# Performance work log

Measured on AMD Instinct MI355X. Metric: run time of the kernel, lower is better.

Reference implementation:

```python
import jax, jax.numpy as jnp
import numpy as np

B, S, E, H = 16, 512, 768, 12
D = E // H
SCALING = 1.0 / np.sqrt(D * 1.0)  # scaling_factor = 1


def setup_inputs() -> dict:
    key = jax.random.key(0)
    ks = jax.random.split(key, 8)
    query = jax.random.normal(ks[0], (B, S, E), dtype=jnp.float32)
    key_in = jax.random.normal(ks[1], (B, S, E), dtype=jnp.float32)
    value = jax.random.normal(ks[2], (B, S, E), dtype=jnp.float32)
    key_padding_mask = jax.random.randint(ks[3], (B, S), 0, 2).astype(jnp.bool_)
    attn_bias = jax.random.normal(ks[4], (B, H, S, S), dtype=jnp.float32)
    # Learned params. NOTE: original code applies wq to q, k AND v (wk/wv unused).
    Wq = jax.random.normal(ks[5], (E, E), dtype=jnp.float32) * (1.0 / np.sqrt(E))
    bq = jnp.zeros((E,), dtype=jnp.float32)
    Wo = jax.random.normal(ks[6], (E, E), dtype=jnp.float32) * (1.0 / np.sqrt(E))
    bo = jnp.zeros((E,), dtype=jnp.float32)
    return {"query": query, "key": key_in, "value": value,
            "key_padding_mask": key_padding_mask, "attn_bias": attn_bias,
            "Wq": Wq, "bq": bq, "Wo": Wo, "bo": bo}


def _split_heads(x):
    # [B,S,E] -> [B,H,S,D]
    return x.reshape(B, S, H, D).transpose(0, 2, 1, 3)


def reference(query, key, value, key_padding_mask, attn_bias, Wq, bq, Wo, bo):
    q = (query @ Wq + bq) * jnp.asarray(SCALING, query.dtype)
    k = key @ Wq + bq      # faithful: wq used for k and v in the source
    v = value @ Wq + bq
    q, k, v = _split_heads(q), _split_heads(k), _split_heads(v)  # [B,H,S,D]
    w = jnp.einsum('bhtd,bhsd->bhts', q, k)                      # [B,H,T,S]
    w = jnp.where(key_padding_mask[:, None, None, :], -jnp.inf, w)
    w = w + attn_bias
    attn = jax.nn.softmax(w, axis=-1)  # dropout is no-op (training=False)
    o = jnp.einsum('bhts,bhsd->bhtd', attn, v)
    o = o.transpose(0, 2, 1, 3).reshape(B, S, E)
    o = o @ Wo + bo
    attn_weights = w.reshape(B * H, S, S)
    return (o, attn_weights, attn.reshape(B * H, S, S))
```

## Files before the change

### kernel.cpp

```cpp
#include <hip/hip_runtime.h>
#include <cmath>

#define BB 16
#define SS 512
#define EE 768
#define HH 12
#define DD 64
#define NBH (BB*HH)

#define MASK_NEG (-1.0e30f)

__device__ __forceinline__ unsigned short bf16_rn(float x) {
    unsigned u = __float_as_uint(x);
    u += 0x7FFFu + ((u >> 16) & 1u);
    return (unsigned short)(u >> 16);
}
__device__ __forceinline__ float bf16_tof(unsigned short h) {
    return __uint_as_float(((unsigned)h) << 16);
}

typedef __attribute__((ext_vector_type(8))) short bf16x8;
typedef __attribute__((ext_vector_type(4))) float f32x4;
typedef __attribute__((ext_vector_type(4))) unsigned short u16x4;

__global__ __launch_bounds__(256) void conv_w_kernel(
    const float* __restrict__ Wq, const float* __restrict__ Wo,
    unsigned short* __restrict__ wtq, unsigned short* __restrict__ wto)
{
    const float* __restrict__ W = blockIdx.z ? Wo : Wq;
    unsigned short* __restrict__ wt = blockIdx.z ? wto : wtq;
    const int k = blockIdx.x * 256 + threadIdx.x;
    const int n = blockIdx.y;
    const float x = W[(size_t)k * EE + n];
    const unsigned short h = bf16_rn(x);
    const float r = x - bf16_tof(h);
    const unsigned short m = bf16_rn(r);
    const float l2 = r - bf16_tof(m);
    const unsigned short l = bf16_rn(l2);
    const size_t PL = (size_t)EE * EE;
    wt[0 * PL + (size_t)n * EE + k] = h;
    wt[1 * PL + (size_t)n * EE + k] = m;
    wt[2 * PL + (size_t)n * EE + k] = l;
}

__global__ __launch_bounds__(256) void split_gemm_qkv_kernel(
    const float* __restrict__ Xq, const float* __restrict__ Xk,
    const float* __restrict__ Xv, const unsigned short* __restrict__ wt,
    const float* __restrict__ bvec,
    unsigned short* __restrict__ qp, unsigned short* __restrict__ kp,
    unsigned short* __restrict__ vtp)
{
    const int z = blockIdx.z;
    const float* __restrict__ X = (z == 1) ? Xk : (z == 2) ? Xv : Xq;
    const float scale = (z == 0) ? 0.125f : 1.0f;

    const int m0 = blockIdx.x * 128;
    const int n0 = blockIdx.y * 128;

    __shared__ __align__(16) unsigned short lds[4 * 4096];
    const int AH = 0, AL = 4096, BH = 8192, BL = 12288;

    const int tid = threadIdx.x;
    const int srow = tid >> 2;
    const int sg   = tid & 3;
    const int wv = tid >> 6;
    const int wr = wv >> 1, wc = wv & 1;
    const int lane = tid & 63;
    const int l15 = lane & 15, lg = lane >> 4;

    const size_t PL = (size_t)EE * EE;
    const size_t PS = (size_t)NBH * SS * DD;

    f32x4 acc[4][4];
#pragma unroll
    for (int i = 0; i < 4; ++i)
#pragma unroll
        for (int j = 0; j < 4; ++j) acc[i][j] = (f32x4){0.f, 0.f, 0.f, 0.f};

#pragma unroll 1
    for (int k0 = 0; k0 < EE; k0 += 32) {
#pragma unroll
        for (int half = 0; half < 2; ++half) {
            const int row = srow + 64 * half;
            const float* xp = &X[(size_t)(m0 + row) * EE + k0 + sg * 8];
            const float4 f0 = *reinterpret_cast<const float4*>(xp);
            const float4 f1 = *reinterpret_cast<const float4*>(xp + 4);
            const float xs[8] = {f0.x, f0.y, f0.z, f0.w, f1.x, f1.y, f1.z, f1.w};
            bf16x8 hv, mv;
#pragma unroll
            for (int e = 0; e < 8; ++e) {
                const float x = xs[e];
                const unsigned short h = bf16_rn(x);
                const unsigned short m = bf16_rn(x - bf16_tof(h));
                hv[e] = (short)h;
                mv[e] = (short)m;
            }
            const int o = row * 32 + sg * 8;
            *reinterpret_cast<bf16x8*>(&lds[AH + o]) = hv;
            *reinterpret_cast<bf16x8*>(&lds[AL + o]) = mv;

            const size_t bo = (size_t)(n0 + row) * EE + k0 + sg * 8;
            *reinterpret_cast<bf16x8*>(&lds[BH + o]) =
                *reinterpret_cast<const bf16x8*>(&wt[0 * PL + bo]);
            *reinterpret_cast<bf16x8*>(&lds[BL + o]) =
                *reinterpret_cast<const bf16x8*>(&wt[1 * PL + bo]);
        }
        __syncthreads();

        bf16x8 ah[4], al[4];
#pragma unroll
        for (int i = 0; i < 4; ++i) {
            const int o = (wr * 64 + i * 16 + l15) * 32 + lg * 8;
            ah[i] = *reinterpret_cast<const bf16x8*>(&lds[AH + o]);
            al[i] = *reinterpret_cast<const bf16x8*>(&lds[AL + o]);
        }
#pragma unroll
        for (int j = 0; j < 4; ++j) {
            const int o = (wc * 64 + j * 16 + l15) * 32 + lg * 8;
            const bf16x8 bh = *reinterpret_cast<const bf16x8*>(&lds[BH + o]);
            const bf16x8 bl = *reinterpret_cast<const bf16x8*>(&lds[BL + o]);
#pragma unroll
            for (int i = 0; i < 4; ++i) {
                acc[i][j] = __builtin_amdgcn_mfma_f32_16x16x32_bf16(ah[i], bh, acc[i][j], 0, 0, 0);
                acc[i][j] = __builtin_amdgcn_mfma_f32_16x16x32_bf16(ah[i], bl, acc[i][j], 0, 0, 0);
                acc[i][j] = __builtin_amdgcn_mfma_f32_16x16x32_bf16(al[i], bh, acc[i][j], 0, 0, 0);
                acc[i][j] = __builtin_amdgcn_mfma_f32_16x16x32_bf16(al[i], bl, acc[i][j], 0, 0, 0);
            }
        }
        __syncthreads();
    }

    unsigned short* __restrict__ dstp = (z == 0) ? qp : kp;
#pragma unroll
    for (int j = 0; j < 4; ++j) {
        const int n = n0 + wc * 64 + j * 16 + l15;
        const float bvn = bvec[n];
        const int h = n >> 6, d = n & 63;
#pragma unroll
        for (int i = 0; i < 4; ++i) {
            const int mb = m0 + wr * 64 + i * 16 + lg * 4;
#pragma unroll
            for (int r = 0; r < 4; ++r) {
                const int m = mb + r;
                const int bh_ = (m >> 9) * HH + h;
                const int srow_ = m & 511;
                const float val = (acc[i][j][r] + bvn) * scale;
                const unsigned short hi = bf16_rn(val);
                const unsigned short lo = bf16_rn(val - bf16_tof(hi));
                if (z == 2) {
                    const size_t o = ((size_t)bh_ * DD + d) * SS + srow_;
                    vtp[o] = hi;
                    vtp[o + PS] = lo;
                } else {
                    const size_t o = ((size_t)bh_ * SS + srow_) * DD + d;
                    dstp[o] = hi;
                    dstp[o + PS] = lo;
                }
            }
        }
    }
}

__global__ __launch_bounds__(256) void flash_attn_kernel(
    const unsigned short* __restrict__ qp, const unsigned short* __restrict__ kp,
    const unsigned short* __restrict__ vt, const unsigned char* __restrict__ mask,
    const float* __restrict__ bias, float* __restrict__ wout,
    float* __restrict__ ohb, float* __restrict__ stat_m,
    float* __restrict__ stat_inv)
{
    const int bh = blockIdx.y;
    const int b = bh / HH, h = bh % HH;
    const int t0 = blockIdx.x * 64;
    const int tid = threadIdx.x;
    const int wv = tid >> 6;
    const int lane = tid & 63, l15 = lane & 15, lg = lane >> 4;
    const size_t PS = (size_t)NBH * SS * DD;

    __shared__ __align__(16) unsigned short kbuf[2 * 64 * 68];
    __shared__ __align__(16) unsigned short vbuf[2 * 64 * 68];
    __shared__ __align__(16) unsigned short pbuf[4 * 2 * 16 * 68];

    bf16x8 bqh[2], bql[2];
    {
        const unsigned short* qbase = &qp[((size_t)bh * SS + t0 + wv * 16) * DD];
#pragma unroll
        for (int kc = 0; kc < 2; ++kc) {
            const size_t o = (size_t)l15 * DD + kc * 32 + lg * 8;
            bqh[kc] = *reinterpret_cast<const bf16x8*>(&qbase[o]);
            bql[kc] = *reinterpret_cast<const bf16x8*>(&qbase[o + PS]);
        }
    }

    float rm = -3.0e38f, rs = 0.0f;

    f32x4 oac[4];
#pragma unroll
    for (int j = 0; j < 4; ++j) oac[j] = (f32x4){0.f, 0.f, 0.f, 0.f};

    const int t = t0 + wv * 16 + l15;

#pragma unroll 1
    for (int c = 0; c < 8; ++c) {
        const int sc = c * 64;
        __syncthreads();

        const unsigned short* kbase = &kp[((size_t)bh * SS + sc) * DD];
        const unsigned short* vbase = &vt[(size_t)bh * DD * SS + sc];
#pragma unroll
        for (int rep = 0; rep < 2; ++rep) {
            const int row = (tid >> 3) + rep * 32;
            const int g = (tid & 7) * 8;
            *reinterpret_cast<bf16x8*>(&kbuf[row * 68 + g]) =
                *reinterpret_cast<const bf16x8*>(&kbase[(size_t)row * DD + g]);
            *reinterpret_cast<bf16x8*>(&kbuf[64 * 68 + row * 68 + g]) =
                *reinterpret_cast<const bf16x8*>(&kbase[(size_t)row * DD + g + PS]);
            *reinterpret_cast<bf16x8*>(&vbuf[row * 68 + g]) =
                *reinterpret_cast<const bf16x8*>(&vbase[(size_t)row * SS + g]);
            *reinterpret_cast<bf16x8*>(&vbuf[64 * 68 + row * 68 + g]) =
                *reinterpret_cast<const bf16x8*>(&vbase[(size_t)row * SS + g + PS]);
        }
        __syncthreads();

        f32x4 ws[4];
#pragma unroll
        for (int i = 0; i < 4; ++i) ws[i] = (f32x4){0.f, 0.f, 0.f, 0.f};
#pragma unroll
        for (int kc = 0; kc < 2; ++kc) {
#pragma unroll
            for (int i = 0; i < 4; ++i) {
                const int o = (i * 16 + l15) * 68 + kc * 32 + lg * 8;
                const bf16x8 ah = *reinterpret_cast<const bf16x8*>(&kbuf[o]);
                const bf16x8 al = *reinterpret_cast<const bf16x8*>(&kbuf[64 * 68 + o]);
                ws[i] = __builtin_amdgcn_mfma_f32_16x16x32_bf16(ah, bqh[kc], ws[i], 0, 0, 0);
                ws[i] = __builtin_amdgcn_mfma_f32_16x16x32_bf16(ah, bql[kc], ws[i], 0, 0, 0);
                ws[i] = __builtin_amdgcn_mfma_f32_16x16x32_bf16(al, bqh[kc], ws[i], 0, 0, 0);
                ws[i] = __builtin_amdgcn_mfma_f32_16x16x32_bf16(al, bql[kc], ws[i], 0, 0, 0);
            }
        }

        float mx = -3.0e38f;
#pragma unroll
        for (int i = 0; i < 4; ++i) {
            const int s = sc + i * 16 + lg * 4;
            const size_t go = ((size_t)bh * SS + t) * SS + s;
            const float4 bv = *reinterpret_cast<const float4*>(&bias[go]);
            const uchar4 mk = *reinterpret_cast<const uchar4*>(&mask[b * SS + s]);
            float4 w4;
            w4.x = mk.x ? MASK_NEG : ws[i][0] + bv.x;
            w4.y = mk.y ? MASK_NEG : ws[i][1] + bv.y;
            w4.z = mk.z ? MASK_NEG : ws[i][2] + bv.z;
            w4.w = mk.w ? MASK_NEG : ws[i][3] + bv.w;
            *reinterpret_cast<float4*>(&wout[go]) = w4;
            ws[i][0] = w4.x; ws[i][1] = w4.y; ws[i][2] = w4.z; ws[i][3] = w4.w;
            mx = fmaxf(mx, fmaxf(fmaxf(w4.x, w4.y), fmaxf(w4.z, w4.w)));
        }
        mx = fmaxf(mx, __shfl_xor(mx, 16));
        mx = fmaxf(mx, __shfl_xor(mx, 32));

        const float m_new = fmaxf(rm, mx);
        float sm = 0.0f;
#pragma unroll
        for (int i = 0; i < 4; ++i)
#pragma unroll
            for (int r = 0; r < 4; ++r) sm += __expf(ws[i][r] - m_new);
        sm += __shfl_xor(sm, 16);
        sm += __shfl_xor(sm, 32);
        const float scl = __expf(rm - m_new);
        rs = rs * scl + sm;
        rm = m_new;

        unsigned short* pw = &pbuf[(wv * 2) * 16 * 68];
#pragma unroll
        for (int i = 0; i < 4; ++i) {
            float4 p4;
            p4.x = __expf(ws[i][0] - m_new);
            p4.y = __expf(ws[i][1] - m_new);
            p4.z = __expf(ws[i][2] - m_new);
            p4.w = __expf(ws[i][3] - m_new);
            u16x4 hv, lv;
            hv.x = bf16_rn(p4.x); lv.x = bf16_rn(p4.x - bf16_tof(hv.x));
            hv.y = bf16_rn(p4.y); lv.y = bf16_rn(p4.y - bf16_tof(hv.y));
            hv.z = bf16_rn(p4.z); lv.z = bf16_rn(p4.z - bf16_tof(hv.z));
            hv.w = bf16_rn(p4.w); lv.w = bf16_rn(p4.w - bf16_tof(hv.w));
            const int po = l15 * 68 + i * 16 + lg * 4;
            *reinterpret_cast<u16x4*>(&pw[po]) = hv;
            *reinterpret_cast<u16x4*>(&pw[16 * 68 + po]) = lv;
        }

        float sclr[4];
#pragma unroll
        for (int r = 0; r < 4; ++r) sclr[r] = __shfl(scl, lg * 4 + r);
#pragma unroll
        for (int j = 0; j < 4; ++j)
#pragma unroll
            for (int r = 0; r < 4; ++r) oac[j][r] *= sclr[r];

#pragma unroll
        for (int kc = 0; kc < 2; ++kc) {
            const int ko = kc * 32 + lg * 8;
            const bf16x8 pah = *reinterpret_cast<const bf16x8*>(&pw[l15 * 68 + ko]);
            const bf16x8 pal = *reinterpret_cast<const bf16x8*>(&pw[16 * 68 + l15 * 68 + ko]);
#pragma unroll
            for (int j = 0; j < 4; ++j) {
                const int o = (j * 16 + l15) * 68 + ko;
                const bf16x8 vh = *reinterpret_cast<const bf16x8*>(&vbuf[o]);
                const bf16x8 vl = *reinterpret_cast<const bf16x8*>(&vbuf[64 * 68 + o]);
                oac[j] = __builtin_amdgcn_mfma_f32_16x16x32_bf16(pah, vh, oac[j], 0, 0, 0);
                oac[j] = __builtin_amdgcn_mfma_f32_16x16x32_bf16(pah, vl, oac[j], 0, 0, 0);
                oac[j] = __builtin_amdgcn_mfma_f32_16x16x32_bf16(pal, vh, oac[j], 0, 0, 0);
                oac[j] = __builtin_amdgcn_mfma_f32_16x16x32_bf16(pal, vl, oac[j], 0, 0, 0);
            }
        }
    }

    const float inv = 1.0f / rs;
    if (lg == 0) {
        stat_m[(size_t)bh * SS + t] = rm;
        stat_inv[(size_t)bh * SS + t] = inv;
    }
    float invr[4];
#pragma unroll
    for (int r = 0; r < 4; ++r) invr[r] = __shfl(inv, lg * 4 + r);
#pragma unroll
    for (int j = 0; j < 4; ++j)
#pragma unroll
        for (int r = 0; r < 4; ++r) {
            const int tr = t0 + wv * 16 + lg * 4 + r;
            ohb[((size_t)b * SS + tr) * EE + h * DD + j * 16 + l15] = oac[j][r] * invr[r];
        }
}

__global__ __launch_bounds__(256) void finish_kernel(
    const float* __restrict__ X, const unsigned short* __restrict__ wt,
    const float* __restrict__ bvec, float* __restrict__ dflat,
    const float* __restrict__ win, const float* __restrict__ stat_m,
    const float* __restrict__ stat_inv, float* __restrict__ attn)
{
    __shared__ __align__(16) unsigned short lds[6 * 4096];

    if (blockIdx.x >= 384) {
        const int nb = gridDim.x - 384;
        const size_t total = (size_t)NBH * SS * (SS / 4);
        for (size_t g = (size_t)(blockIdx.x - 384) * 256 + threadIdx.x; g < total;
             g += (size_t)nb * 256) {
            const size_t row = g >> 7;
            const float m_ = stat_m[row];
            const float iv = stat_inv[row];
            const float4 w4 = reinterpret_cast<const float4*>(win)[g];
            float4 p4;
            p4.x = __expf(w4.x - m_) * iv;
            p4.y = __expf(w4.y - m_) * iv;
            p4.z = __expf(w4.z - m_) * iv;
            p4.w = __expf(w4.w - m_) * iv;
            reinterpret_cast<float4*>(attn)[g] = p4;
        }
        return;
    }

    const int m0 = (blockIdx.x & 63) * 128;
    const int n0 = (blockIdx.x >> 6) * 128;

    const int AH = 0, AM = 4096, AL = 8192, BH = 12288, BM = 16384, BL = 20480;

    const int tid = threadIdx.x;
    const int srow = tid >> 2;
    const int sg   = tid & 3;
    const int wv = tid >> 6;
    const int wr = wv >> 1, wc = wv & 1;
    const int lane = tid & 63;
    const int l15 = lane & 15, lg = lane >> 4;
    const size_t PL = (size_t)EE * EE;

    f32x4 acc[4][4];
#pragma unroll
    for (int i = 0; i < 4; ++i)
#pragma unroll
        for (int j = 0; j < 4; ++j) acc[i][j] = (f32x4){0.f, 0.f, 0.f, 0.f};

#pragma unroll 1
    for (int k0 = 0; k0 < EE; k0 += 32) {
#pragma unroll
        for (int half = 0; half < 2; ++half) {
            const int row = srow + 64 * half;
            const float* xp = &X[(size_t)(m0 + row) * EE + k0 + sg * 8];
            const float4 f0 = *reinterpret_cast<const float4*>(xp);
            const float4 f1 = *reinterpret_cast<const float4*>(xp + 4);
            const float xs[8] = {f0.x, f0.y, f0.z, f0.w, f1.x, f1.y, f1.z, f1.w};
            bf16x8 hv, mv, lv;
#pragma unroll
            for (int e = 0; e < 8; ++e) {
                const float x = xs[e];
                const unsigned short h = bf16_rn(x);
                const float r = x - bf16_tof(h);
                const unsigned short m = bf16_rn(r);
                const float l2 = r - bf16_tof(m);
                hv[e] = (short)h;
                mv[e] = (short)m;
                lv[e] = (short)bf16_rn(l2);
            }
            const int o = row * 32 + sg * 8;
            *reinterpret_cast<bf16x8*>(&lds[AH + o]) = hv;
            *reinterpret_cast<bf16x8*>(&lds[AM + o]) = mv;
            *reinterpret_cast<bf16x8*>(&lds[AL + o]) = lv;

            const size_t bo = (size_t)(n0 + row) * EE + k0 + sg * 8;
            *reinterpret_cast<bf16x8*>(&lds[BH + o]) =
                *reinterpret_cast<const bf16x8*>(&wt[0 * PL + bo]);
            *reinterpret_cast<bf16x8*>(&lds[BM + o]) =
                *reinterpret_cast<const bf16x8*>(&wt[1 * PL + bo]);
            *reinterpret_cast<bf16x8*>(&lds[BL + o]) =
                *reinterpret_cast<const bf16x8*>(&wt[2 * PL + bo]);
        }
        __syncthreads();

        bf16x8 ah[4], am[4], al[4];
#pragma unroll
        for (int i = 0; i < 4; ++i) {
            const int o = (wr * 64 + i * 16 + l15) * 32 + lg * 8;
            ah[i] = *reinterpret_cast<const bf16x8*>(&lds[AH + o]);
            am[i] = *reinterpret_cast<const bf16x8*>(&lds[AM + o]);
            al[i] = *reinterpret_cast<const bf16x8*>(&lds[AL + o]);
        }
#pragma unroll
        for (int j = 0; j < 4; ++j) {
            const int o = (wc * 64 + j * 16 + l15) * 32 + lg * 8;
            const bf16x8 bh = *reinterpret_cast<const bf16x8*>(&lds[BH + o]);
            const bf16x8 bm = *reinterpret_cast<const bf16x8*>(&lds[BM + o]);
            const bf16x8 bl = *reinterpret_cast<const bf16x8*>(&lds[BL + o]);
#pragma unroll
            for (int i = 0; i < 4; ++i) {
                acc[i][j] = __builtin_amdgcn_mfma_f32_16x16x32_bf16(ah[i], bh, acc[i][j], 0, 0, 0);
                acc[i][j] = __builtin_amdgcn_mfma_f32_16x16x32_bf16(ah[i], bm, acc[i][j], 0, 0, 0);
                acc[i][j] = __builtin_amdgcn_mfma_f32_16x16x32_bf16(am[i], bh, acc[i][j], 0, 0, 0);
                acc[i][j] = __builtin_amdgcn_mfma_f32_16x16x32_bf16(ah[i], bl, acc[i][j], 0, 0, 0);
                acc[i][j] = __builtin_amdgcn_mfma_f32_16x16x32_bf16(al[i], bh, acc[i][j], 0, 0, 0);
                acc[i][j] = __builtin_amdgcn_mfma_f32_16x16x32_bf16(am[i], bm, acc[i][j], 0, 0, 0);
            }
        }
        __syncthreads();
    }

#pragma unroll
    for (int j = 0; j < 4; ++j) {
        const int n = n0 + wc * 64 + j * 16 + l15;
        const float bvn = bvec[n];
#pragma unroll
        for (int i = 0; i < 4; ++i) {
            const int mb = m0 + wr * 64 + i * 16 + lg * 4;
#pragma unroll
            for (int r = 0; r < 4; ++r)
                dflat[(size_t)(mb + r) * EE + n] = acc[i][j][r] + bvn;
        }
    }
}

__global__ __launch_bounds__(256) void proj_kernel(
    const float* __restrict__ Xq, const float* __restrict__ Xk,
    const float* __restrict__ Xv, const float* __restrict__ W,
    const float* __restrict__ bvec, float* __restrict__ qb,
    float* __restrict__ kb, float* __restrict__ vb)
{
    const int z = blockIdx.z;
    const float* __restrict__ X = (z == 0) ? Xq : (z == 1) ? Xk : Xv;
    float* __restrict__ Dst = (z == 0) ? qb : (z == 1) ? kb : vb;
    const float scale = (z == 0) ? 0.125f : 1.0f;

    const int m0 = blockIdx.x * 128;
    const int n0 = blockIdx.y * 128;

    __shared__ float As[16][128];
    __shared__ float Bs[16][128];

    const int tid = threadIdx.x;
    const int ty = tid >> 4, tx = tid & 15;

    float acc[8][8];
#pragma unroll
    for (int i = 0; i < 8; ++i)
#pragma unroll
        for (int j = 0; j < 8; ++j) acc[i][j] = 0.0f;

    const int arow = tid >> 1;
    const int ak   = (tid & 1) * 8;
    const int brow = tid >> 4;
    const int bn   = (tid & 15) * 8;

    for (int k0 = 0; k0 < EE; k0 += 16) {
        const float4* ap = reinterpret_cast<const float4*>(&X[(size_t)(m0 + arow) * EE + k0 + ak]);
        float4 a0 = ap[0], a1 = ap[1];
        As[ak + 0][arow] = a0.x; As[ak + 1][arow] = a0.y;
        As[ak + 2][arow] = a0.z; As[ak + 3][arow] = a0.w;
        As[ak + 4][arow] = a1.x; As[ak + 5][arow] = a1.y;
        As[ak + 6][arow] = a1.z; As[ak + 7][arow] = a1.w;

        const float4* bp = reinterpret_cast<const float4*>(&W[(size_t)(k0 + brow) * EE + n0 + bn]);
        float4 b0 = bp[0], b1 = bp[1];
        *reinterpret_cast<float4*>(&Bs[brow][bn])     = b0;
        *reinterpret_cast<float4*>(&Bs[brow][bn + 4]) = b1;
        __syncthreads();

#pragma unroll
        for (int kk = 0; kk < 16; ++kk) {
            float4 aA = *reinterpret_cast<const float4*>(&As[kk][ty * 8]);
            float4 aB = *reinterpret_cast<const float4*>(&As[kk][ty * 8 + 4]);
            float4 bA = *reinterpret_cast<const float4*>(&Bs[kk][tx * 8]);
            float4 bB = *reinterpret_cast<const float4*>(&Bs[kk][tx * 8 + 4]);
            float av[8] = {aA.x, aA.y, aA.z, aA.w, aB.x, aB.y, aB.z, aB.w};
            float bv[8] = {bA.x, bA.y, bA.z, bA.w, bB.x, bB.y, bB.z, bB.w};
#pragma unroll
            for (int i = 0; i < 8; ++i)
#pragma unroll
                for (int j = 0; j < 8; ++j)
                    acc[i][j] = fmaf(av[i], bv[j], acc[i][j]);
        }
        __syncthreads();
    }

    const int nbase = n0 + tx * 8;
    float bq8[8];
    {
        float4 c0 = *reinterpret_cast<const float4*>(&bvec[nbase]);
        float4 c1 = *reinterpret_cast<const float4*>(&bvec[nbase + 4]);
        bq8[0]=c0.x; bq8[1]=c0.y; bq8[2]=c0.z; bq8[3]=c0.w;
        bq8[4]=c1.x; bq8[5]=c1.y; bq8[6]=c1.z; bq8[7]=c1.w;
    }
    const int hh = nbase >> 6;
    const int dd = nbase & 63;
#pragma unroll
    for (int i = 0; i < 8; ++i) {
        const int m = m0 + ty * 8 + i;
        const int bidx = m >> 9;
        const int srow = m & 511;
        float* dst = &Dst[(((size_t)bidx * HH + hh) * SS + srow) * DD + dd];
        float4 v0, v1;
        v0.x = (acc[i][0] + bq8[0]) * scale;
        v0.y = (acc[i][1] + bq8[1]) * scale;
        v0.z = (acc[i][2] + bq8[2]) * scale;
        v0.w = (acc[i][3] + bq8[3]) * scale;
        v1.x = (acc[i][4] + bq8[4]) * scale;
        v1.y = (acc[i][5] + bq8[5]) * scale;
        v1.z = (acc[i][6] + bq8[6]) * scale;
        v1.w = (acc[i][7] + bq8[7]) * scale;
        *reinterpret_cast<float4*>(dst)     = v0;
        *reinterpret_cast<float4*>(dst + 4) = v1;
    }
}

__global__ __launch_bounds__(256) void scores_kernel(
    const float* __restrict__ qb, const float* __restrict__ kb,
    const unsigned char* __restrict__ mask,
    const float* __restrict__ bias, float* __restrict__ wout)
{
    const int bh = blockIdx.z;
    const int b  = bh / HH;
    const int t0 = blockIdx.y * 128;
    const int s0 = blockIdx.x * 128;

    __shared__ float As[16][128];
    __shared__ float Bs[16][128];

    const int tid = threadIdx.x;
    const int ty = tid >> 4, tx = tid & 15;

    float acc[8][8];
#pragma unroll
    for (int i = 0; i < 8; ++i)
#pragma unroll
        for (int j = 0; j < 8; ++j) acc[i][j] = 0.0f;

    const int arow = tid >> 1;
    const int ak   = (tid & 1) * 8;

    const float* __restrict__ qbase = &qb[(size_t)bh * SS * DD];
    const float* __restrict__ kbase = &kb[(size_t)bh * SS * DD];

    for (int k0 = 0; k0 < DD; k0 += 16) {
        const float4* ap = reinterpret_cast<const float4*>(&qbase[(size_t)(t0 + arow) * DD + k0 + ak]);
        float4 a0 = ap[0], a1 = ap[1];
        As[ak + 0][arow] = a0.x; As[ak + 1][arow] = a0.y;
        As[ak + 2][arow] = a0.z; As[ak + 3][arow] = a0.w;
        As[ak + 4][arow] = a1.x; As[ak + 5][arow] = a1.y;
        As[ak + 6][arow] = a1.z; As[ak + 7][arow] = a1.w;

        const float4* bp = reinterpret_cast<const float4*>(&kbase[(size_t)(s0 + arow) * DD + k0 + ak]);
        float4 b0 = bp[0], b1 = bp[1];
        Bs[ak + 0][arow] = b0.x; Bs[ak + 1][arow] = b0.y;
        Bs[ak + 2][arow] = b0.z; Bs[ak + 3][arow] = b0.w;
        Bs[ak + 4][arow] = b1.x; Bs[ak + 5][arow] = b1.y;
        Bs[ak + 6][arow] = b1.z; Bs[ak + 7][arow] = b1.w;
        __syncthreads();

#pragma unroll
        for (int kk = 0; kk < 16; ++kk) {
            float4 aA = *reinterpret_cast<const float4*>(&As[kk][ty * 8]);
            float4 aB = *reinterpret_cast<const float4*>(&As[kk][ty * 8 + 4]);
            float4 bA = *reinterpret_cast<const float4*>(&Bs[kk][tx * 8]);
            float4 bB = *reinterpret_cast<const float4*>(&Bs[kk][tx * 8 + 4]);
            float av[8] = {aA.x, aA.y, aA.z, aA.w, aB.x, aB.y, aB.z, aB.w};
            float bv[8] = {bA.x, bA.y, bA.z, bA.w, bB.x, bB.y, bB.z, bB.w};
#pragma unroll
            for (int i = 0; i < 8; ++i)
#pragma unroll
                for (int j = 0; j < 8; ++j)
                    acc[i][j] = fmaf(av[i], bv[j], acc[i][j]);
        }
        __syncthreads();
    }

    const int scol = s0 + tx * 8;
    const uint2 mv = *reinterpret_cast<const uint2*>(&mask[b * SS + scol]);
    bool msk[8];
    msk[0] = (mv.x & 0x000000ffu) != 0;
    msk[1] = (mv.x & 0x0000ff00u) != 0;
    msk[2] = (mv.x & 0x00ff0000u) != 0;
    msk[3] = (mv.x & 0xff000000u) != 0;
    msk[4] = (mv.y & 0x000000ffu) != 0;
    msk[5] = (mv.y & 0x0000ff00u) != 0;
    msk[6] = (mv.y & 0x00ff0000u) != 0;
    msk[7] = (mv.y & 0xff000000u) != 0;
#pragma unroll
    for (int i = 0; i < 8; ++i) {
        const int t = t0 + ty * 8 + i;
        const float4 bv0 = *reinterpret_cast<const float4*>(&bias[((size_t)bh * SS + t) * SS + scol]);
        const float4 bv1 = *reinterpret_cast<const float4*>(&bias[((size_t)bh * SS + t) * SS + scol + 4]);
        float4 w0, w1;
        w0.x = msk[0] ? MASK_NEG : acc[i][0] + bv0.x;
        w0.y = msk[1] ? MASK_NEG : acc[i][1] + bv0.y;
        w0.z = msk[2] ? MASK_NEG : acc[i][2] + bv0.z;
        w0.w = msk[3] ? MASK_NEG : acc[i][3] + bv0.w;
        w1.x = msk[4] ? MASK_NEG : acc[i][4] + bv1.x;
        w1.y = msk[5] ? MASK_NEG : acc[i][5] + bv1.y;
        w1.z = msk[6] ? MASK_NEG : acc[i][6] + bv1.z;
        w1.w = msk[7] ? MASK_NEG : acc[i][7] + bv1.w;
        float* wrow = &wout[((size_t)bh * SS + t) * SS + scol];
        *reinterpret_cast<float4*>(wrow)     = w0;
        *reinterpret_cast<float4*>(wrow + 4) = w1;
    }
}

__global__ __launch_bounds__(256) void softmax_pv_kernel(
    const float* __restrict__ win, const float* __restrict__ vb,
    float* __restrict__ attn, float* __restrict__ ohb)
{
    const int bh = blockIdx.y;
    const int b = bh / HH, h = bh % HH;
    const int t0 = blockIdx.x * 64;
    const int wave = threadIdx.x >> 6;
    const int lane = threadIdx.x & 63;

    __shared__ float pws[4][8][512];

#pragma unroll 1
    for (int g = 0; g < 2; ++g) {
        const int tb = t0 + wave * 16 + g * 8;

#pragma unroll 1
        for (int r = 0; r < 8; ++r) {
            const int t = tb + r;
            const float4* wp = reinterpret_cast<const float4*>(&win[((size_t)bh * SS + t) * SS + lane * 8]);
            float4 w0 = wp[0], w1 = wp[1];
            float wv[8] = {w0.x,w0.y,w0.z,w0.w,w1.x,w1.y,w1.z,w1.w};
            float mx = wv[0];
#pragma unroll
            for (int j = 1; j < 8; ++j) mx = fmaxf(mx, wv[j]);
#pragma unroll
            for (int off = 32; off > 0; off >>= 1)
                mx = fmaxf(mx, __shfl_xor(mx, off));
            float e[8];
            float sum = 0.0f;
#pragma unroll
            for (int j = 0; j < 8; ++j) { e[j] = __expf(wv[j] - mx); sum += e[j]; }
#pragma unroll
            for (int off = 32; off > 0; off >>= 1)
                sum += __shfl_xor(sum, off);
            const float inv = 1.0f / sum;
            float4 p0, p1;
            p0.x = e[0]*inv; p0.y = e[1]*inv; p0.z = e[2]*inv; p0.w = e[3]*inv;
            p1.x = e[4]*inv; p1.y = e[5]*inv; p1.z = e[6]*inv; p1.w = e[7]*inv;
            float* arow = &attn[((size_t)bh * SS + t) * SS + lane * 8];
            *reinterpret_cast<float4*>(arow)     = p0;
            *reinterpret_cast<float4*>(arow + 4) = p1;
            *reinterpret_cast<float4*>(&pws[wave][r][lane * 8])     = p0;
            *reinterpret_cast<float4*>(&pws[wave][r][lane * 8 + 4]) = p1;
        }
        __syncthreads();

        float oacc[8] = {0,0,0,0,0,0,0,0};
#pragma unroll 2
        for (int s = 0; s < SS; s += 4) {
            const float v0 = vb[((size_t)bh * SS + s + 0) * DD + lane];
            const float v1 = vb[((size_t)bh * SS + s + 1) * DD + lane];
            const float v2 = vb[((size_t)bh * SS + s + 2) * DD + lane];
            const float v3 = vb[((size_t)bh * SS + s + 3) * DD + lane];
#pragma unroll
            for (int r = 0; r < 8; ++r) {
                const float4 p4 = *reinterpret_cast<const float4*>(&pws[wave][r][s]);
                oacc[r] = fmaf(p4.x, v0, oacc[r]);
                oacc[r] = fmaf(p4.y, v1, oacc[r]);
                oacc[r] = fmaf(p4.z, v2, oacc[r]);
                oacc[r] = fmaf(p4.w, v3, oacc[r]);
            }
        }
#pragma unroll
        for (int r = 0; r < 8; ++r)
            ohb[((size_t)b * SS + tb + r) * EE + h * DD + lane] = oacc[r];
        __syncthreads();
    }
}

__global__ __launch_bounds__(256) void outproj_kernel(
    const float* __restrict__ A, const float* __restrict__ W,
    const float* __restrict__ bvec, float* __restrict__ out)
{
    const int m0 = blockIdx.x * 128;
    const int n0 = blockIdx.y * 128;

    __shared__ float As[16][128];
    __shared__ float Bs[16][128];

    const int tid = threadIdx.x;
    const int ty = tid >> 4, tx = tid & 15;

    float acc[8][8];
#pragma unroll
    for (int i = 0; i < 8; ++i)
#pragma unroll
        for (int j = 0; j < 8; ++j) acc[i][j] = 0.0f;

    const int arow = tid >> 1;
    const int ak   = (tid & 1) * 8;
    const int brow = tid >> 4;
    const int bn   = (tid & 15) * 8;

    for (int k0 = 0; k0 < EE; k0 += 16) {
        const float4* ap = reinterpret_cast<const float4*>(&A[(size_t)(m0 + arow) * EE + k0 + ak]);
        float4 a0 = ap[0], a1 = ap[1];
        As[ak + 0][arow] = a0.x; As[ak + 1][arow] = a0.y;
        As[ak + 2][arow] = a0.z; As[ak + 3][arow] = a0.w;
        As[ak + 4][arow] = a1.x; As[ak + 5][arow] = a1.y;
        As[ak + 6][arow] = a1.z; As[ak + 7][arow] = a1.w;

        const float4* bp = reinterpret_cast<const float4*>(&W[(size_t)(k0 + brow) * EE + n0 + bn]);
        float4 b0 = bp[0], b1 = bp[1];
        *reinterpret_cast<float4*>(&Bs[brow][bn])     = b0;
        *reinterpret_cast<float4*>(&Bs[brow][bn + 4]) = b1;
        __syncthreads();

#pragma unroll
        for (int kk = 0; kk < 16; ++kk) {
            float4 aA = *reinterpret_cast<const float4*>(&As[kk][ty * 8]);
            float4 aB = *reinterpret_cast<const float4*>(&As[kk][ty * 8 + 4]);
            float4 bA = *reinterpret_cast<const float4*>(&Bs[kk][tx * 8]);
            float4 bB = *reinterpret_cast<const float4*>(&Bs[kk][tx * 8 + 4]);
            float av[8] = {aA.x, aA.y, aA.z, aA.w, aB.x, aB.y, aB.z, aB.w};
            float bv[8] = {bA.x, bA.y, bA.z, bA.w, bB.x, bB.y, bB.z, bB.w};
#pragma unroll
            for (int i = 0; i < 8; ++i)
#pragma unroll
                for (int j = 0; j < 8; ++j)
                    acc[i][j] = fmaf(av[i], bv[j], acc[i][j]);
        }
        __syncthreads();
    }

    const int nbase = n0 + tx * 8;
    float bq8[8];
    {
        float4 c0 = *reinterpret_cast<const float4*>(&bvec[nbase]);
        float4 c1 = *reinterpret_cast<const float4*>(&bvec[nbase + 4]);
        bq8[0]=c0.x; bq8[1]=c0.y; bq8[2]=c0.z; bq8[3]=c0.w;
        bq8[4]=c1.x; bq8[5]=c1.y; bq8[6]=c1.z; bq8[7]=c1.w;
    }
#pragma unroll
    for (int i = 0; i < 8; ++i) {
        const int m = m0 + ty * 8 + i;
        float* dst = &out[(size_t)m * EE + nbase];
        float4 v0, v1;
        v0.x = acc[i][0] + bq8[0]; v0.y = acc[i][1] + bq8[1];
        v0.z = acc[i][2] + bq8[2]; v0.w = acc[i][3] + bq8[3];
        v1.x = acc[i][4] + bq8[4]; v1.y = acc[i][5] + bq8[5];
        v1.z = acc[i][6] + bq8[6]; v1.w = acc[i][7] + bq8[7];
        *reinterpret_cast<float4*>(dst)     = v0;
        *reinterpret_cast<float4*>(dst + 4) = v1;
    }
}

extern "C" void kernel_launch(void* const* d_in, const int* in_sizes, int n_in,
                              void* d_out, int out_size, void* d_ws, size_t ws_size,
                              hipStream_t stream)
{
    const float* query = (const float*)d_in[0];
    const float* key   = (const float*)d_in[1];
    const float* value = (const float*)d_in[2];
    const unsigned char* mask = (const unsigned char*)d_in[3];
    const float* bias  = (const float*)d_in[4];
    const float* Wq    = (const float*)d_in[5];
    const float* bq    = (const float*)d_in[6];
    const float* Wo    = (const float*)d_in[7];
    const float* bo    = (const float*)d_in[8];

    float* out_o = (float*)d_out;
    float* out_w = out_o + (size_t)BB * SS * EE;
    float* out_a = out_w + (size_t)NBH * SS * SS;

    const size_t headsz = (size_t)NBH * SS * DD;
    const size_t wt_elems = 3 * (size_t)EE * EE;

    const size_t need_mfma = 3 * (2 * headsz * sizeof(unsigned short))
                           + headsz * sizeof(float)
                           + 2 * wt_elems * sizeof(unsigned short);

    if (ws_size >= need_mfma) {
        unsigned short* qp = (unsigned short*)d_ws;
        unsigned short* kp = qp + 2 * headsz;
        unsigned short* vt = kp + 2 * headsz;
        float* ohb = (float*)(vt + 2 * headsz);
        unsigned short* wtq = (unsigned short*)(ohb + headsz);
        unsigned short* wto = wtq + wt_elems;
        float* stat_m   = (float*)wtq;
        float* stat_inv = stat_m + (size_t)NBH * SS;

        conv_w_kernel<<<dim3(3, EE, 2), 256, 0, stream>>>(Wq, Wo, wtq, wto);
        split_gemm_qkv_kernel<<<dim3(64, 6, 3), 256, 0, stream>>>(
            query, key, value, wtq, bq, qp, kp, vt);
        flash_attn_kernel<<<dim3(8, NBH), 256, 0, stream>>>(
            qp, kp, vt, mask, bias, out_w, ohb, stat_m, stat_inv);
        finish_kernel<<<384 + 2048, 256, 0, stream>>>(
            ohb, wto, bo, out_o, out_w, stat_m, stat_inv, out_a);
    } else {
        const size_t base_bytes = 4 * headsz * sizeof(float);
        if (ws_size < base_bytes) return;
        float* qb  = (float*)d_ws;
        float* kb  = qb + headsz;
        float* vb  = kb + headsz;
        float* ohb = vb + headsz;
        proj_kernel<<<dim3(64, 6, 3), 256, 0, stream>>>(query, key, value, Wq, bq, qb, kb, vb);
        scores_kernel<<<dim3(4, 4, NBH), 256, 0, stream>>>(qb, kb, mask, bias, out_w);
        softmax_pv_kernel<<<dim3(8, NBH), 256, 0, stream>>>(out_w, vb, out_a, ohb);
        outproj_kernel<<<dim3(64, 6), 256, 0, stream>>>(ohb, Wo, bo, out_o);
    }
}
```

Measured before the change: 498.8 us.

## Prefetch next K-tile into registers in QKV GEMM and flash-attention loops

```diff
diff --git a/kernel.cpp b/kernel.cpp
--- a/kernel.cpp
+++ b/kernel.cpp
@@ -77,15 +77,33 @@
 #pragma unroll
         for (int j = 0; j < 4; ++j) acc[i][j] = (f32x4){0.f, 0.f, 0.f, 0.f};
 
+    float4 xf[2][2];
+    bf16x8 wh[2], wl[2];
+
+#define QKV_LOAD(K0)                                                          \
+    {                                                                         \
+        _Pragma("unroll")                                                     \
+        for (int half = 0; half < 2; ++half) {                                \
+            const int row = srow + 64 * half;                                 \
+            const float* xp = &X[(size_t)(m0 + row) * EE + (K0) + sg * 8];    \
+            xf[half][0] = *reinterpret_cast<const float4*>(xp);               \
+            xf[half][1] = *reinterpret_cast<const float4*>(xp + 4);           \
+            const size_t bo = (size_t)(n0 + row) * EE + (K0) + sg * 8;        \
+            wh[half] = *reinterpret_cast<const bf16x8*>(&wt[0 * PL + bo]);    \
+            wl[half] = *reinterpret_cast<const bf16x8*>(&wt[1 * PL + bo]);    \
+        }                                                                     \
+    }
+
+    QKV_LOAD(0);
+
 #pragma unroll 1
     for (int k0 = 0; k0 < EE; k0 += 32) {
+        __syncthreads();
 #pragma unroll
         for (int half = 0; half < 2; ++half) {
             const int row = srow + 64 * half;
-            const float* xp = &X[(size_t)(m0 + row) * EE + k0 + sg * 8];
-            const float4 f0 = *reinterpret_cast<const float4*>(xp);
-            const float4 f1 = *reinterpret_cast<const float4*>(xp + 4);
-            const float xs[8] = {f0.x, f0.y, f0.z, f0.w, f1.x, f1.y, f1.z, f1.w};
+            const float xs[8] = {xf[half][0].x, xf[half][0].y, xf[half][0].z, xf[half][0].w,
+                                 xf[half][1].x, xf[half][1].y, xf[half][1].z, xf[half][1].w};
             bf16x8 hv, mv;
 #pragma unroll
             for (int e = 0; e < 8; ++e) {
@@ -98,14 +116,12 @@
             const int o = row * 32 + sg * 8;
             *reinterpret_cast<bf16x8*>(&lds[AH + o]) = hv;
             *reinterpret_cast<bf16x8*>(&lds[AL + o]) = mv;
-
-            const size_t bo = (size_t)(n0 + row) * EE + k0 + sg * 8;
-            *reinterpret_cast<bf16x8*>(&lds[BH + o]) =
-                *reinterpret_cast<const bf16x8*>(&wt[0 * PL + bo]);
-            *reinterpret_cast<bf16x8*>(&lds[BL + o]) =
-                *reinterpret_cast<const bf16x8*>(&wt[1 * PL + bo]);
-        }
-        __syncthreads();
+            *reinterpret_cast<bf16x8*>(&lds[BH + o]) = wh[half];
+            *reinterpret_cast<bf16x8*>(&lds[BL + o]) = wl[half];
+        }
+        __syncthreads();
+
+        if (k0 + 32 < EE) QKV_LOAD(k0 + 32);
 
         bf16x8 ah[4], al[4];
 #pragma unroll
@@ -127,8 +143,8 @@
                 acc[i][j] = __builtin_amdgcn_mfma_f32_16x16x32_bf16(al[i], bl, acc[i][j], 0, 0, 0);
             }
         }
-        __syncthreads();
-    }
+    }
+#undef QKV_LOAD
 
     unsigned short* __restrict__ dstp = (z == 0) ? qp : kp;
 #pragma unroll
@@ -199,27 +215,55 @@
 
     const int t = t0 + wv * 16 + l15;
 
+    const unsigned short* __restrict__ kb0 = &kp[(size_t)bh * SS * DD];
+    const unsigned short* __restrict__ vb0 = &vt[(size_t)bh * DD * SS];
+    const int srow2 = tid >> 3, sg2 = (tid & 7) * 8;
+
+    bf16x8 krh[2], krl[2], vrh[2], vrl[2];
+
+#define FA_LOADKV(SC)                                                         \
+    {                                                                         \
+        _Pragma("unroll")                                                     \
+        for (int rep = 0; rep < 2; ++rep) {                                   \
+            const int row = srow2 + rep * 32;                                 \
+            krh[rep] = *reinterpret_cast<const bf16x8*>(                      \
+                &kb0[(size_t)((SC) + row) * DD + sg2]);                       \
+            krl[rep] = *reinterpret_cast<const bf16x8*>(                      \
+                &kb0[(size_t)((SC) + row) * DD + sg2 + PS]);                  \
+            vrh[rep] = *reinterpret_cast<const bf16x8*>(                      \
+                &vb0[(size_t)row * SS + (SC) + sg2]);                         \
+            vrl[rep] = *reinterpret_cast<const bf16x8*>(                      \
+                &vb0[(size_t)row * SS + (SC) + sg2 + PS]);                    \
+        }                                                                     \
+    }
+
+    FA_LOADKV(0);
+
 #pragma unroll 1
     for (int c = 0; c < 8; ++c) {
         const int sc = c * 64;
         __syncthreads();
 
-        const unsigned short* kbase = &kp[((size_t)bh * SS + sc) * DD];
-        const unsigned short* vbase = &vt[(size_t)bh * DD * SS + sc];
 #pragma unroll
         for (int rep = 0; rep < 2; ++rep) {
-            const int row = (tid >> 3) + rep * 32;
-            const int g = (tid & 7) * 8;
-            *reinterpret_cast<bf16x8*>(&kbuf[row * 68 + g]) =
-                *reinterpret_cast<const bf16x8*>(&kbase[(size_t)row * DD + g]);
-            *reinterpret_cast<bf16x8*>(&kbuf[64 * 68 + row * 68 + g]) =
-                *reinterpret_cast<const bf16x8*>(&kbase[(size_t)row * DD + g + PS]);
-            *reinterpret_cast<bf16x8*>(&vbuf[row * 68 + g]) =
-                *reinterpret_cast<const bf16x8*>(&vbase[(size_t)row * SS + g]);
-            *reinterpret_cast<bf16x8*>(&vbuf[64 * 68 + row * 68 + g]) =
-                *reinterpret_cast<const bf16x8*>(&vbase[(size_t)row * SS + g + PS]);
-        }
-        __syncthreads();
+            const int row = srow2 + rep * 32;
+            *reinterpret_cast<bf16x8*>(&kbuf[row * 68 + sg2]) = krh[rep];
+            *reinterpret_cast<bf16x8*>(&kbuf[64 * 68 + row * 68 + sg2]) = krl[rep];
+            *reinterpret_cast<bf16x8*>(&vbuf[row * 68 + sg2]) = vrh[rep];
+            *reinterpret_cast<bf16x8*>(&vbuf[64 * 68 + row * 68 + sg2]) = vrl[rep];
+        }
+        __syncthreads();
+
+        if (c < 7) FA_LOADKV(sc + 64);
+
+        float4 bvr[4];
+        uchar4 mkr[4];
+#pragma unroll
+        for (int i = 0; i < 4; ++i) {
+            const int s = sc + i * 16 + lg * 4;
+            bvr[i] = *reinterpret_cast<const float4*>(&bias[((size_t)bh * SS + t) * SS + s]);
+            mkr[i] = *reinterpret_cast<const uchar4*>(&mask[b * SS + s]);
+        }
 
         f32x4 ws[4];
 #pragma unroll
@@ -243,13 +287,11 @@
         for (int i = 0; i < 4; ++i) {
             const int s = sc + i * 16 + lg * 4;
             const size_t go = ((size_t)bh * SS + t) * SS + s;
-            const float4 bv = *reinterpret_cast<const float4*>(&bias[go]);
-            const uchar4 mk = *reinterpret_cast<const uchar4*>(&mask[b * SS + s]);
             float4 w4;
-            w4.x = mk.x ? MASK_NEG : ws[i][0] + bv.x;
-            w4.y = mk.y ? MASK_NEG : ws[i][1] + bv.y;
-            w4.z = mk.z ? MASK_NEG : ws[i][2] + bv.z;
-            w4.w = mk.w ? MASK_NEG : ws[i][3] + bv.w;
+            w4.x = mkr[i].x ? MASK_NEG : ws[i][0] + bvr[i].x;
+            w4.y = mkr[i].y ? MASK_NEG : ws[i][1] + bvr[i].y;
+            w4.z = mkr[i].z ? MASK_NEG : ws[i][2] + bvr[i].z;
+            w4.w = mkr[i].w ? MASK_NEG : ws[i][3] + bvr[i].w;
             *reinterpret_cast<float4*>(&wout[go]) = w4;
             ws[i][0] = w4.x; ws[i][1] = w4.y; ws[i][2] = w4.z; ws[i][3] = w4.w;
             mx = fmaxf(mx, fmaxf(fmaxf(w4.x, w4.y), fmaxf(w4.z, w4.w)));
@@ -312,6 +354,7 @@
             }
         }
     }
+#undef FA_LOADKV
 
     const float inv = 1.0f / rs;
     if (lg == 0) {
```

Result: faster. 439.1 us (-12.0%).
